# Kernel tuning notes

Measured on AMD Instinct MI355X. Metric: run time of the kernel, lower is better.

The kernel has to match this reference:

```python
import jax, jax.numpy as jnp
import numpy as np

N = 16384      # nodes
E = 131072     # edges
L = 256        # latent size
H = 256        # mlp hidden size
S = 4          # message passing steps
OUT = 128      # decoder node output size
EPS = 1e-6     # flax LayerNorm epsilon


def _mlp(x, W0, b0, W1, b1):
    h = jax.nn.relu(x @ W0 + b0)
    return h @ W1 + b1


def _mlp_ln(x, W0, b0, W1, b1, ls, lb):
    y = _mlp(x, W0, b0, W1, b1)
    mu = y.mean(-1, keepdims=True)
    var = ((y - mu) ** 2).mean(-1, keepdims=True)
    return (y - mu) * jax.lax.rsqrt(var + EPS) * ls + lb


def setup_inputs() -> dict:
    key = jax.random.key(0)
    ks = iter(jax.random.split(key, 64))
    std = 0.02

    def w(shape):
        return jax.random.normal(next(ks), shape, dtype=jnp.float32) * std

    inp = {
        'node_feats': jax.random.normal(next(ks), (N, 3), dtype=jnp.float32),
        'edge_feats': jax.random.normal(next(ks), (E, 4), dtype=jnp.float32),
        'senders': jax.random.randint(next(ks), (E,), 0, N, dtype=jnp.int32),
        'receivers': jax.random.randint(next(ks), (E,), 0, N, dtype=jnp.int32),
        # node embedder MLP (3 -> H -> L) + LayerNorm
        'en_W0': w((3, H)), 'en_b0': jnp.zeros((H,)), 'en_W1': w((H, L)), 'en_b1': jnp.zeros((L,)),
        'en_ls': jnp.ones((L,)), 'en_lb': jnp.zeros((L,)),
        # edge embedder MLP (4 -> H -> L) + LayerNorm
        'ee_W0': w((4, H)), 'ee_b0': jnp.zeros((H,)), 'ee_W1': w((H, L)), 'ee_b1': jnp.zeros((L,)),
        'ee_ls': jnp.ones((L,)), 'ee_lb': jnp.zeros((L,)),
        # processor edge MLPs, stacked over S steps (3L -> H -> L) + LN
        'pe_W0': w((S, 3 * L, H)), 'pe_b0': jnp.zeros((S, H)), 'pe_W1': w((S, H, L)), 'pe_b1': jnp.zeros((S, L)),
        'pe_ls': jnp.ones((S, L)), 'pe_lb': jnp.zeros((S, L)),
        # processor node MLPs, stacked over S steps (2L -> H -> L) + LN
        'pn_W0': w((S, 2 * L, H)), 'pn_b0': jnp.zeros((S, H)), 'pn_W1': w((S, H, L)), 'pn_b1': jnp.zeros((S, L)),
        'pn_ls': jnp.ones((S, L)), 'pn_lb': jnp.zeros((S, L)),
        # node decoder MLP (L -> H -> OUT), no LayerNorm
        'dn_W0': w((L, H)), 'dn_b0': jnp.zeros((H,)), 'dn_W1': w((H, OUT)), 'dn_b1': jnp.zeros((OUT,)),
    }
    return inp


def reference(node_feats, edge_feats, senders, receivers,
              en_W0, en_b0, en_W1, en_b1, en_ls, en_lb,
              ee_W0, ee_b0, ee_W1, ee_b1, ee_ls, ee_lb,
              pe_W0, pe_b0, pe_W1, pe_b1, pe_ls, pe_lb,
              pn_W0, pn_b0, pn_W1, pn_b1, pn_ls, pn_lb,
              dn_W0, dn_b0, dn_W1, dn_b1):
    # Embed raw node/edge features into latent space.
    nodes = _mlp_ln(node_feats, en_W0, en_b0, en_W1, en_b1, en_ls, en_lb)   # [N, L]
    edges = _mlp_ln(edge_feats, ee_W0, ee_b0, ee_W1, ee_b1, ee_ls, ee_lb)   # [E, L]

    def step(carry, p):
        nodes, edges = carry
        (eW0, eb0, eW1, eb1, els, elb, nW0, nb0, nW1, nb1, nls, nlb) = p
        # Edge update: MLP on [edge, sender_node, receiver_node].
        ein = jnp.concatenate([edges, nodes[senders], nodes[receivers]], axis=-1)  # [E, 3L]
        new_e = _mlp_ln(ein, eW0, eb0, eW1, eb1, els, elb)                          # [E, L]
        # Aggregate new edge messages into receiver nodes (segment_sum).
        agg = jax.ops.segment_sum(new_e, receivers, num_segments=N)                # [N, L]
        # Node update: MLP on [node, aggregated messages].
        nin = jnp.concatenate([nodes, agg], axis=-1)                                # [N, 2L]
        new_n = _mlp_ln(nin, nW0, nb0, nW1, nb1, nls, nlb)                          # [N, L]
        # Residual connections (as in DeepTypedGraphNet processor).
        return (nodes + new_n, edges + new_e), None

    (nodes, edges), _ = jax.lax.scan(
        step, (nodes, edges),
        (pe_W0, pe_b0, pe_W1, pe_b1, pe_ls, pe_lb,
         pn_W0, pn_b0, pn_W1, pn_b1, pn_ls, pn_lb))

    # Decoder on nodes (no LayerNorm on the output head).
    out = _mlp(nodes, dn_W0, dn_b0, dn_W1, dn_b1)  # [N, OUT]
    return out
```

## Files before the change

kernel.cpp:

```cpp
#include <hip/hip_runtime.h>
#include <hip/hip_bf16.h>

#define NN 16384
#define NE 131072
#define L 256
#define SSTEPS 4
#define OUTD 128

typedef __attribute__((ext_vector_type(8))) short bf16x8;
typedef __attribute__((ext_vector_type(4))) float f32x4;

typedef const unsigned __attribute__((address_space(1)))* as1_u32p;
typedef unsigned __attribute__((address_space(3)))* as3_u32p;

__device__ __forceinline__ void gload16(const void* g, void* lds) {
  __builtin_amdgcn_global_load_lds((as1_u32p)g, (as3_u32p)lds, 16, 0, 0);
}

__device__ __forceinline__ short f2bs(float f) {
  unsigned u = __builtin_bit_cast(unsigned, f);
  u = (u + 0x7fffu + ((u >> 16) & 1u)) >> 16;
  return (short)u;
}
__device__ __forceinline__ float bs2f(short s) {
  unsigned u = ((unsigned)(unsigned short)s) << 16;
  return __builtin_bit_cast(float, u);
}
__device__ __forceinline__ unsigned cvt_pk_bf16(float lo, float hi) {
  unsigned r;
  asm("v_cvt_pk_bf16_f32 %0, %1, %2" : "=v"(r) : "v"(lo), "v"(hi));
  return r;
}
__device__ __forceinline__ bf16x8 pack_bf16x8(const float v[8]) {
  union { unsigned u[4]; bf16x8 b; } r;
#pragma unroll
  for (int k = 0; k < 4; ++k) r.u[k] = cvt_pk_bf16(v[2 * k], v[2 * k + 1]);
  return r.b;
}

__device__ __forceinline__ void store_tile(short* hs, int l, int mi, int nb,
                                           f32x4 v) {
  const int lm = l & 15, g = l >> 4;
#pragma unroll
  for (int i = 0; i < 4; ++i) {
    const float part = __shfl_xor(v[i], 1);
    if ((l & 1) == 0) {
      const int row = mi * 16 + g * 4 + i;
      const int col = nb + lm;
      const int off = (row * 512 + col * 2) ^ ((row & 7) << 4);
      *(unsigned*)((char*)hs + off) = cvt_pk_bf16(v[i], part);
    }
  }
}

template <int MI, int NT, int KC, int AST>
__device__ __forceinline__ void gemm_lds(const short* __restrict__ Wp,
                                         int Ncols, const short* hs, int n0,
                                         int l, f32x4 acc[MI][NT]) {
  const int lm = l & 15, g = l >> 4;
#pragma unroll
  for (int kc = 0; kc < KC; ++kc) {
    bf16x8 a[MI];
#pragma unroll
    for (int mi = 0; mi < MI; ++mi) {
      const int row = mi * 16 + lm;
      const int off = (row * AST + kc * 64 + g * 16) ^ ((row & 7) << 4);
      a[mi] = *(const bf16x8*)((const char*)hs + off);
    }
#pragma unroll
    for (int ni = 0; ni < NT; ++ni) {
      const int n = n0 + ni * 16 + lm;
      bf16x8 b = *(const bf16x8*)(Wp + ((size_t)kc * Ncols + n) * 32 + g * 8);
#pragma unroll
      for (int mi = 0; mi < MI; ++mi)
        acc[mi][ni] =
            __builtin_amdgcn_mfma_f32_16x16x32_bf16(a[mi], b, acc[mi][ni], 0, 0, 0);
    }
  }
}

__global__ void pack_w(const float* __restrict__ src, short* __restrict__ dst,
                       int K, int N, int cnt) {
  const size_t total = (size_t)K * N * cnt;
  for (size_t i = (size_t)blockIdx.x * blockDim.x + threadIdx.x; i < total;
       i += (size_t)gridDim.x * blockDim.x) {
    const size_t mat = i / ((size_t)K * N);
    const int rem = (int)(i - mat * (size_t)K * N);
    const int k = rem / N, n = rem - k * N;
    dst[mat * (size_t)K * N + ((size_t)(k >> 5) * N + n) * 32 + (k & 31)] =
        f2bs(src[i]);
  }
}

__global__ void pack_w0_pad(const float* __restrict__ src,
                            short* __restrict__ dst, int Kreal) {
  const int i = blockIdx.x * 256 + threadIdx.x;
  if (i >= 256 * 32) return;
  const int n = i >> 5, k = i & 31;
  dst[n * 32 + k] = (k < Kreal) ? f2bs(src[k * 256 + n]) : (short)0;
}

__device__ __forceinline__ void stage_tile256(const short* __restrict__ src0,
                                              short* As, int w, int l) {
#pragma unroll
  for (int i = 0; i < 4; ++i) {
    const int rbase = w * 8 + i * 2;
    const int r = rbase + (l >> 5);
    const int boff = ((l & 31) * 16) ^ ((r & 7) << 4);
    gload16((const char*)(src0 + (size_t)r * L) + boff, As + rbase * 256);
  }
}

__device__ __forceinline__ void stage_tile512(const short* __restrict__ a_src,
                                              const short* __restrict__ b_src,
                                              short* As, int w, int l, int n0) {
#pragma unroll
  for (int i = 0; i < 8; ++i) {
    const int r = w * 8 + i;
    const int cb = (l * 16) ^ ((r & 7) << 4);
    const int cs = cb >> 1;
    const short* src = (cs < 256)
                           ? a_src + (size_t)(n0 + r) * L + cs
                           : b_src + (size_t)(n0 + r) * L + (cs - 256);
    gload16(src, As + r * 512);
  }
}

__global__ void csr_hist(const int* __restrict__ recv, int* __restrict__ deg) {
  const int e = blockIdx.x * 256 + threadIdx.x;
  atomicAdd(&deg[recv[e]], 1);
}
__global__ __launch_bounds__(256) void csr_scan(const int* __restrict__ deg,
                                                int* __restrict__ start,
                                                int* __restrict__ cursor) {
  __shared__ int part[256];
  const int t = threadIdx.x;
  int s = 0;
  for (int i = 0; i < NN / 256; ++i) s += deg[t * (NN / 256) + i];
  part[t] = s;
  __syncthreads();
  if (t == 0) {
    int acc = 0;
    for (int i = 0; i < 256; ++i) {
      const int v = part[i];
      part[i] = acc;
      acc += v;
    }
  }
  __syncthreads();
  int acc = part[t];
  for (int i = 0; i < NN / 256; ++i) {
    const int n = t * (NN / 256) + i;
    start[n] = acc;
    cursor[n] = acc;
    acc += deg[n];
  }
  if (t == 255) start[NN] = acc;
}
__global__ void csr_scatter(const int* __restrict__ recv,
                            int* __restrict__ cursor, int* __restrict__ elist) {
  const int e = blockIdx.x * 256 + threadIdx.x;
  const int p = atomicAdd(&cursor[recv[e]], 1);
  elist[p] = e;
}
__global__ void csr_sort(const int* __restrict__ start, int* __restrict__ elist) {
  const int n = blockIdx.x * blockDim.x + threadIdx.x;
  if (n >= NN) return;
  const int b = start[n], e = start[n + 1];
  for (int i = b + 1; i < e; ++i) {
    const int v = elist[i];
    int j = i - 1;
    while (j >= b && elist[j] > v) {
      elist[j + 1] = elist[j];
      --j;
    }
    elist[j + 1] = v;
  }
}

__global__ __launch_bounds__(256) void agg_gather(
    const short* __restrict__ new_e, const int* __restrict__ start,
    const int* __restrict__ elist, short* __restrict__ agg_b) {
  const int t = threadIdx.x, w = t >> 6, l = t & 63;
  const int half = l >> 5, lc = l & 31;
  const int n0 = blockIdx.x * 64;
  for (int i = 0; i < 8; ++i) {
    const int n = n0 + w * 16 + i * 2 + half;
    const int b = start[n], e = start[n + 1];
    float acc[8] = {0.f, 0.f, 0.f, 0.f, 0.f, 0.f, 0.f, 0.f};
#pragma unroll 2
    for (int j = b; j < e; ++j) {
      const int eid = elist[j];
      const bf16x8 v = *(const bf16x8*)(new_e + (size_t)eid * L + lc * 8);
#pragma unroll
      for (int k = 0; k < 8; ++k) acc[k] += bs2f(v[k]);
    }
    *(bf16x8*)(agg_b + (size_t)n * L + lc * 8) = pack_bf16x8(acc);
  }
}

__device__ __forceinline__ void ln_row(const short* smem, int row, int seg,
                                       const float lsv[16], const float lbv[16],
                                       float ne[16]) {
  const int off0 = (row * 512 + seg * 16) ^ ((row & 7) << 4);
  const int off1 = (row * 512 + 256 + seg * 16) ^ ((row & 7) << 4);
  const bf16x8 y0 = *(const bf16x8*)((const char*)smem + off0);
  const bf16x8 y1 = *(const bf16x8*)((const char*)smem + off1);
  float v[16];
#pragma unroll
  for (int k = 0; k < 8; ++k) {
    v[k] = bs2f(y0[k]);
    v[8 + k] = bs2f(y1[k]);
  }
  float s = 0.f;
#pragma unroll
  for (int k = 0; k < 16; ++k) s += v[k];
#pragma unroll
  for (int o = 1; o < 16; o <<= 1) s += __shfl_xor(s, o);
  const float mu = s * (1.f / 256.f);
  float sq = 0.f;
#pragma unroll
  for (int k = 0; k < 16; ++k) {
    const float d = v[k] - mu;
    sq += d * d;
  }
#pragma unroll
  for (int o = 1; o < 16; o <<= 1) sq += __shfl_xor(sq, o);
  const float rstd = rsqrtf(sq * (1.f / 256.f) + 1e-6f);
#pragma unroll
  for (int k = 0; k < 16; ++k) ne[k] = (v[k] - mu) * rstd * lsv[k] + lbv[k];
}

__device__ __forceinline__ void load16(const float* __restrict__ p, int seg,
                                       float d[16]) {
  const float4 a0 = *(const float4*)(p + seg * 8);
  const float4 a1 = *(const float4*)(p + seg * 8 + 4);
  const float4 a2 = *(const float4*)(p + 128 + seg * 8);
  const float4 a3 = *(const float4*)(p + 128 + seg * 8 + 4);
  d[0] = a0.x; d[1] = a0.y; d[2] = a0.z; d[3] = a0.w;
  d[4] = a1.x; d[5] = a1.y; d[6] = a1.z; d[7] = a1.w;
  d[8] = a2.x; d[9] = a2.y; d[10] = a2.z; d[11] = a2.w;
  d[12] = a3.x; d[13] = a3.y; d[14] = a3.z; d[15] = a3.w;
}

__global__ __launch_bounds__(256, 4) void proj_mfma(
    const short* __restrict__ nodes_b, const short* __restrict__ Wfull,
    short* __restrict__ NSb, short* __restrict__ NRb) {
  __shared__ char smem[16384];
  short* As = (short*)smem;
  const int t = threadIdx.x, w = t >> 6, l = t & 63;
  const int tr = t >> 4, seg = t & 15;
  const int n0 = blockIdx.x * 32;
  const short* Wp = Wfull + (size_t)(8 + blockIdx.y * 8) * 256 * 32;
  short* out = blockIdx.y ? NRb : NSb;

  stage_tile256(nodes_b + (size_t)n0 * L, As, w, l);
  __syncthreads();

  f32x4 acc[2][4] = {};
  gemm_lds<2, 4, 8, 512>(Wp, L, As, w * 64, l, acc);
  __syncthreads();
#pragma unroll
  for (int ni = 0; ni < 4; ++ni)
#pragma unroll
    for (int mi = 0; mi < 2; ++mi)
      store_tile(As, l, mi, w * 64 + ni * 16, acc[mi][ni]);
  __syncthreads();

#pragma unroll
  for (int p = 0; p < 2; ++p) {
    const int row = p * 16 + tr;
    const int off0 = (row * 512 + seg * 16) ^ ((row & 7) << 4);
    const int off1 = (row * 512 + 256 + seg * 16) ^ ((row & 7) << 4);
    const bf16x8 y0 = *(const bf16x8*)((const char*)As + off0);
    const bf16x8 y1 = *(const bf16x8*)((const char*)As + off1);
    *(bf16x8*)(out + (size_t)(n0 + row) * L + seg * 8) = y0;
    *(bf16x8*)(out + (size_t)(n0 + row) * L + 128 + seg * 8) = y1;
  }
}

__global__ __launch_bounds__(256, 3) void edge_step_mfma(
    const short* __restrict__ NSb, const short* __restrict__ NRb,
    short* __restrict__ edges_b, short* __restrict__ new_e,
    const int* __restrict__ senders, const int* __restrict__ receivers,
    const short* __restrict__ W0p, const float* __restrict__ b0,
    const short* __restrict__ W1p, const float* __restrict__ b1,
    const float* __restrict__ ls, const float* __restrict__ lb) {
  __shared__ char smem[49152];
  float* nsrf = (float*)smem;
  short* As = (short*)(smem + 32768);
  short* yb = (short*)smem;
  const int t = threadIdx.x, w = t >> 6, l = t & 63;
  const int lm = l & 15, g = l >> 4;
  const int tr = t >> 4, seg = t & 15;
  const int e0 = blockIdx.x * 32;

  const int sn0 = senders[e0 + tr], rc0 = receivers[e0 + tr];
  const int sn1 = senders[e0 + 16 + tr], rc1 = receivers[e0 + 16 + tr];
  stage_tile256(edges_b + (size_t)e0 * L, As, w, l);
  __syncthreads();

  bf16x8 gn[2][2], gr[2][2];
  {
    const short* p0 = NSb + (size_t)sn0 * L + seg * 8;
    gn[0][0] = *(const bf16x8*)p0;
    gn[0][1] = *(const bf16x8*)(p0 + 128);
    const short* p1 = NSb + (size_t)sn1 * L + seg * 8;
    gn[1][0] = *(const bf16x8*)p1;
    gn[1][1] = *(const bf16x8*)(p1 + 128);
    const short* q0 = NRb + (size_t)rc0 * L + seg * 8;
    gr[0][0] = *(const bf16x8*)q0;
    gr[0][1] = *(const bf16x8*)(q0 + 128);
    const short* q1 = NRb + (size_t)rc1 * L + seg * 8;
    gr[1][0] = *(const bf16x8*)q1;
    gr[1][1] = *(const bf16x8*)(q1 + 128);
  }

  f32x4 acc[2][4] = {};
  gemm_lds<2, 4, 8, 512>(W0p, L, As, w * 64, l, acc);

  bf16x8 old0[2], old1[2];
#pragma unroll
  for (int p = 0; p < 2; ++p) {
    const int row = p * 16 + tr;
    old0[p] = *(const bf16x8*)((const char*)As +
                               ((row * 512 + seg * 16) ^ ((row & 7) << 4)));
    old1[p] = *(const bf16x8*)((const char*)As +
                               ((row * 512 + 256 + seg * 16) ^ ((row & 7) << 4)));
  }

#pragma unroll
  for (int p = 0; p < 2; ++p) {
    const int row = p * 16 + tr;
    float s[16];
#pragma unroll
    for (int k = 0; k < 8; ++k) {
      s[k] = bs2f(gn[p][0][k]) + bs2f(gr[p][0][k]);
      s[8 + k] = bs2f(gn[p][1][k]) + bs2f(gr[p][1][k]);
    }
    float* d = nsrf + row * 256 + seg * 8;
    *(float4*)d = make_float4(s[0], s[1], s[2], s[3]);
    *(float4*)(d + 4) = make_float4(s[4], s[5], s[6], s[7]);
    float* d2 = nsrf + row * 256 + 128 + seg * 8;
    *(float4*)d2 = make_float4(s[8], s[9], s[10], s[11]);
    *(float4*)(d2 + 4) = make_float4(s[12], s[13], s[14], s[15]);
  }
  __syncthreads();

#pragma unroll
  for (int ni = 0; ni < 4; ++ni) {
    const float bia = b0[w * 64 + ni * 16 + lm];
    const int col = w * 64 + ni * 16 + lm;
#pragma unroll
    for (int mi = 0; mi < 2; ++mi) {
      f32x4 v = acc[mi][ni];
#pragma unroll
      for (int i = 0; i < 4; ++i) {
        const int row = mi * 16 + g * 4 + i;
        v[i] = fmaxf(v[i] + bia + nsrf[row * 256 + col], 0.f);
      }
      store_tile(As, l, mi, w * 64 + ni * 16, v);
    }
  }
  __syncthreads();

  f32x4 acc2[2][4] = {};
  gemm_lds<2, 4, 8, 512>(W1p, L, As, w * 64, l, acc2);
  __syncthreads();

#pragma unroll
  for (int ni = 0; ni < 4; ++ni) {
    const float bia = b1[w * 64 + ni * 16 + lm];
#pragma unroll
    for (int mi = 0; mi < 2; ++mi) {
      f32x4 v = acc2[mi][ni];
#pragma unroll
      for (int i = 0; i < 4; ++i) v[i] += bia;
      store_tile(yb, l, mi, w * 64 + ni * 16, v);
    }
  }
  __syncthreads();

  float lsv[16], lbv[16];
  load16(ls, seg, lsv);
  load16(lb, seg, lbv);
#pragma unroll
  for (int p = 0; p < 2; ++p) {
    const int row = p * 16 + tr;
    float ne[16];
    ln_row(yb, row, seg, lsv, lbv, ne);
    const size_t e = (size_t)(e0 + row);
    *(bf16x8*)(new_e + e * L + seg * 8) = pack_bf16x8(ne);
    *(bf16x8*)(new_e + e * L + 128 + seg * 8) = pack_bf16x8(ne + 8);
    float r0[8], r1[8];
#pragma unroll
    for (int k = 0; k < 8; ++k) {
      r0[k] = bs2f(old0[p][k]) + ne[k];
      r1[k] = bs2f(old1[p][k]) + ne[8 + k];
    }
    *(bf16x8*)(edges_b + e * L + seg * 8) = pack_bf16x8(r0);
    *(bf16x8*)(edges_b + e * L + 128 + seg * 8) = pack_bf16x8(r1);
  }
}

__global__ __launch_bounds__(256, 4) void node_step_mfma(
    float* __restrict__ nodes_f, short* __restrict__ nodes_b,
    const short* __restrict__ agg_b, const short* __restrict__ W0p,
    const float* __restrict__ b0, const short* __restrict__ W1p,
    const float* __restrict__ b1, const float* __restrict__ ls,
    const float* __restrict__ lb) {
  __shared__ char smem[32768];
  short* As = (short*)smem;
  short* hb = (short*)smem;
  short* yb = (short*)(smem + 16384);
  const int t = threadIdx.x, w = t >> 6, l = t & 63;
  const int lm = l & 15;
  const int tr = t >> 4, seg = t & 15;
  const int n0 = blockIdx.x * 32;

  stage_tile512(nodes_b, agg_b, As, w, l, n0);
  __syncthreads();

  f32x4 acc[2][4] = {};
  gemm_lds<2, 4, 16, 1024>(W0p, L, As, w * 64, l, acc);
  __syncthreads();

#pragma unroll
  for (int ni = 0; ni < 4; ++ni) {
    const float bia = b0[w * 64 + ni * 16 + lm];
#pragma unroll
    for (int mi = 0; mi < 2; ++mi) {
      f32x4 v = acc[mi][ni];
#pragma unroll
      for (int i = 0; i < 4; ++i) v[i] = fmaxf(v[i] + bia, 0.f);
      store_tile(hb, l, mi, w * 64 + ni * 16, v);
    }
  }
  __syncthreads();

  f32x4 acc2[2][4] = {};
  gemm_lds<2, 4, 8, 512>(W1p, L, hb, w * 64, l, acc2);
  __syncthreads();
#pragma unroll
  for (int ni = 0; ni < 4; ++ni) {
    const float bia = b1[w * 64 + ni * 16 + lm];
#pragma unroll
    for (int mi = 0; mi < 2; ++mi) {
      f32x4 v = acc2[mi][ni];
#pragma unroll
      for (int i = 0; i < 4; ++i) v[i] += bia;
      store_tile(yb, l, mi, w * 64 + ni * 16, v);
    }
  }
  __syncthreads();

  float lsv[16], lbv[16];
  load16(ls, seg, lsv);
  load16(lb, seg, lbv);
#pragma unroll
  for (int p = 0; p < 2; ++p) {
    const int row = p * 16 + tr;
    float ne[16];
    ln_row(yb, row, seg, lsv, lbv, ne);
    const size_t n = (size_t)(n0 + row);
    float* nf = nodes_f + n * L;
    float fv[16];
    load16(nf, seg, fv);
    float nv[16];
#pragma unroll
    for (int k = 0; k < 16; ++k) nv[k] = fv[k] + ne[k];
    *(float4*)(nf + seg * 8) = make_float4(nv[0], nv[1], nv[2], nv[3]);
    *(float4*)(nf + seg * 8 + 4) = make_float4(nv[4], nv[5], nv[6], nv[7]);
    *(float4*)(nf + 128 + seg * 8) = make_float4(nv[8], nv[9], nv[10], nv[11]);
    *(float4*)(nf + 128 + seg * 8 + 4) = make_float4(nv[12], nv[13], nv[14], nv[15]);
    *(bf16x8*)(nodes_b + n * L + seg * 8) = pack_bf16x8(nv);
    *(bf16x8*)(nodes_b + n * L + 128 + seg * 8) = pack_bf16x8(nv + 8);
  }
}

template <int K1, bool WF32>
__global__ __launch_bounds__(256) void embed_mfma(
    const float* __restrict__ x, const short* __restrict__ W0p,
    const float* __restrict__ b0, const short* __restrict__ W1p,
    const float* __restrict__ b1, const float* __restrict__ ls,
    const float* __restrict__ lb, float* __restrict__ dst_f,
    short* __restrict__ dst_b) {
  __shared__ short hs[64 * 256];
  __shared__ short xsb[64 * 32];
  const int t = threadIdx.x, w = t >> 6, l = t & 63;
  const int lm = l & 15, g = l >> 4;
  const int tr = t >> 4, seg = t & 15;
  const int r0 = blockIdx.x * 64;

  if (t < 64) {
    const float* xr = x + (size_t)(r0 + t) * K1;
    float v[8] = {0.f, 0.f, 0.f, 0.f, 0.f, 0.f, 0.f, 0.f};
#pragma unroll
    for (int k = 0; k < K1; ++k) v[k] = xr[k];
    bf16x8 z;
#pragma unroll
    for (int k = 0; k < 8; ++k) z[k] = 0;
    char* rb = (char*)xsb + t * 64;
    *(bf16x8*)(rb + (0 ^ ((t & 3) << 4))) = pack_bf16x8(v);
#pragma unroll
    for (int gi = 1; gi < 4; ++gi) *(bf16x8*)(rb + ((gi * 16) ^ ((t & 3) << 4))) = z;
  }
  __syncthreads();

  f32x4 acc[4][4] = {};
  {
    bf16x8 a[4];
#pragma unroll
    for (int mi = 0; mi < 4; ++mi) {
      const int row = mi * 16 + lm;
      a[mi] = *(const bf16x8*)((const char*)xsb + row * 64 +
                               ((g * 16) ^ ((row & 3) << 4)));
    }
#pragma unroll
    for (int ni = 0; ni < 4; ++ni) {
      const int n = w * 64 + ni * 16 + lm;
      bf16x8 b = *(const bf16x8*)(W0p + n * 32 + g * 8);
#pragma unroll
      for (int mi = 0; mi < 4; ++mi)
        acc[mi][ni] =
            __builtin_amdgcn_mfma_f32_16x16x32_bf16(a[mi], b, acc[mi][ni], 0, 0, 0);
    }
  }
#pragma unroll
  for (int ni = 0; ni < 4; ++ni) {
    const float bia = b0[w * 64 + ni * 16 + lm];
#pragma unroll
    for (int mi = 0; mi < 4; ++mi) {
      f32x4 v = acc[mi][ni];
#pragma unroll
      for (int i = 0; i < 4; ++i) v[i] = fmaxf(v[i] + bia, 0.f);
      store_tile(hs, l, mi, w * 64 + ni * 16, v);
    }
  }
  __syncthreads();

  f32x4 acc2[4][4] = {};
  gemm_lds<4, 4, 8, 512>(W1p, L, hs, w * 64, l, acc2);
  __syncthreads();
#pragma unroll
  for (int ni = 0; ni < 4; ++ni) {
    const float bia = b1[w * 64 + ni * 16 + lm];
#pragma unroll
    for (int mi = 0; mi < 4; ++mi) {
      f32x4 v = acc2[mi][ni];
#pragma unroll
      for (int i = 0; i < 4; ++i) v[i] += bia;
      store_tile(hs, l, mi, w * 64 + ni * 16, v);
    }
  }
  __syncthreads();

  float lsv[16], lbv[16];
  load16(ls, seg, lsv);
  load16(lb, seg, lbv);
#pragma unroll
  for (int p = 0; p < 4; ++p) {
    const int row = p * 16 + tr;
    float ne[16];
    ln_row(hs, row, seg, lsv, lbv, ne);
    const size_t n = (size_t)(r0 + row);
    *(bf16x8*)(dst_b + n * L + seg * 8) = pack_bf16x8(ne);
    *(bf16x8*)(dst_b + n * L + 128 + seg * 8) = pack_bf16x8(ne + 8);
    if (WF32) {
      float* df = dst_f + n * L;
      *(float4*)(df + seg * 8) = make_float4(ne[0], ne[1], ne[2], ne[3]);
      *(float4*)(df + seg * 8 + 4) = make_float4(ne[4], ne[5], ne[6], ne[7]);
      *(float4*)(df + 128 + seg * 8) = make_float4(ne[8], ne[9], ne[10], ne[11]);
      *(float4*)(df + 128 + seg * 8 + 4) =
          make_float4(ne[12], ne[13], ne[14], ne[15]);
    }
  }
}

__global__ __launch_bounds__(256) void decoder_mfma(
    const short* __restrict__ nodes_b, const short* __restrict__ W0p,
    const float* __restrict__ b0, const short* __restrict__ W1p,
    const float* __restrict__ b1, float* __restrict__ out) {
  __shared__ short hs[64 * 256];
  const int t = threadIdx.x, w = t >> 6, l = t & 63;
  const int lm = l & 15, g = l >> 4;
  const int n0 = blockIdx.x * 64;

  const short* baseA[4];
#pragma unroll
  for (int mi = 0; mi < 4; ++mi)
    baseA[mi] = nodes_b + (size_t)(n0 + mi * 16 + lm) * L;

  f32x4 acc[4][4] = {};
#pragma unroll
  for (int kc = 0; kc < 8; ++kc) {
    const int koff = kc * 32 + g * 8;
    bf16x8 a[4];
#pragma unroll
    for (int mi = 0; mi < 4; ++mi) a[mi] = *(const bf16x8*)(baseA[mi] + koff);
#pragma unroll
    for (int ni = 0; ni < 4; ++ni) {
      const int n = w * 64 + ni * 16 + lm;
      bf16x8 b = *(const bf16x8*)(W0p + ((size_t)kc * L + n) * 32 + g * 8);
#pragma unroll
      for (int mi = 0; mi < 4; ++mi)
        acc[mi][ni] = __builtin_amdgcn_mfma_f32_16x16x32_bf16(a[mi], b,
                                                             acc[mi][ni],
                                                             0, 0, 0);
    }
  }
#pragma unroll
  for (int ni = 0; ni < 4; ++ni) {
    const float bia = b0[w * 64 + ni * 16 + lm];
#pragma unroll
    for (int mi = 0; mi < 4; ++mi) {
      f32x4 v = acc[mi][ni];
#pragma unroll
      for (int i = 0; i < 4; ++i) v[i] = fmaxf(v[i] + bia, 0.f);
      store_tile(hs, l, mi, w * 64 + ni * 16, v);
    }
  }
  __syncthreads();

  f32x4 acc2[4][2] = {};
  gemm_lds<4, 2, 8, 512>(W1p, OUTD, hs, w * 32, l, acc2);

  float b14[2];
#pragma unroll
  for (int ni = 0; ni < 2; ++ni) b14[ni] = b1[w * 32 + ni * 16 + lm];
#pragma unroll
  for (int mi = 0; mi < 4; ++mi)
#pragma unroll
    for (int ni = 0; ni < 2; ++ni)
#pragma unroll
      for (int i = 0; i < 4; ++i) {
        const int row = n0 + mi * 16 + g * 4 + i;
        const int col = w * 32 + ni * 16 + lm;
        out[(size_t)row * OUTD + col] = acc2[mi][ni][i] + b14[ni];
      }
}

extern "C" void kernel_launch(void* const* d_in, const int* in_sizes, int n_in,
                              void* d_out, int out_size, void* d_ws,
                              size_t ws_size, hipStream_t stream) {
  const float* node_feats = (const float*)d_in[0];
  const float* edge_feats = (const float*)d_in[1];
  const int* senders = (const int*)d_in[2];
  const int* receivers = (const int*)d_in[3];
  auto f = [&](int i) { return (const float*)d_in[i]; };

  char* p = (char*)d_ws;
  auto alloc = [&](size_t bytes) {
    char* q = p;
    p += (bytes + 255) & ~(size_t)255;
    return q;
  };
  float* nodes_f = (float*)alloc((size_t)NN * L * 4);
  short* nodes_b = (short*)alloc((size_t)NN * L * 2);
  short* edges_b = (short*)alloc((size_t)NE * L * 2);
  short* new_e = (short*)alloc((size_t)NE * L * 2);
  short* agg_b = (short*)alloc((size_t)NN * L * 2);
  short* NSb = (short*)alloc((size_t)NN * L * 2);
  short* NRb = (short*)alloc((size_t)NN * L * 2);
  int* deg = (int*)alloc((size_t)NN * 4);
  int* start = (int*)alloc((size_t)(NN + 16) * 4);
  int* cursor = (int*)alloc((size_t)NN * 4);
  int* elist = (int*)alloc((size_t)NE * 4);
  short* en_W0p = (short*)alloc(256 * 32 * 2);
  short* ee_W0p = (short*)alloc(256 * 32 * 2);
  short* en_W1p = (short*)alloc(65536 * 2);
  short* ee_W1p = (short*)alloc(65536 * 2);
  short* pe_W0p = (short*)alloc((size_t)4 * 768 * 256 * 2);
  short* pe_W1p = (short*)alloc((size_t)4 * 65536 * 2);
  short* pn_W0p = (short*)alloc((size_t)4 * 512 * 256 * 2);
  short* pn_W1p = (short*)alloc((size_t)4 * 65536 * 2);
  short* dn_W0p = (short*)alloc(65536 * 2);
  short* dn_W1p = (short*)alloc(32768 * 2);

  hipMemsetAsync(deg, 0, (size_t)NN * 4, stream);
  csr_hist<<<NE / 256, 256, 0, stream>>>(receivers, deg);
  csr_scan<<<1, 256, 0, stream>>>(deg, start, cursor);
  csr_scatter<<<NE / 256, 256, 0, stream>>>(receivers, cursor, elist);
  csr_sort<<<NN / 256, 256, 0, stream>>>(start, elist);

  pack_w0_pad<<<32, 256, 0, stream>>>(f(4), en_W0p, 3);
  pack_w0_pad<<<32, 256, 0, stream>>>(f(10), ee_W0p, 4);
  pack_w<<<256, 256, 0, stream>>>(f(6), en_W1p, 256, 256, 1);
  pack_w<<<256, 256, 0, stream>>>(f(12), ee_W1p, 256, 256, 1);
  pack_w<<<1024, 256, 0, stream>>>(f(16), pe_W0p, 768, 256, 4);
  pack_w<<<512, 256, 0, stream>>>(f(18), pe_W1p, 256, 256, 4);
  pack_w<<<1024, 256, 0, stream>>>(f(22), pn_W0p, 512, 256, 4);
  pack_w<<<512, 256, 0, stream>>>(f(24), pn_W1p, 256, 256, 4);
  pack_w<<<256, 256, 0, stream>>>(f(28), dn_W0p, 256, 256, 1);
  pack_w<<<128, 256, 0, stream>>>(f(30), dn_W1p, 256, 128, 1);

  embed_mfma<3, true><<<NN / 64, 256, 0, stream>>>(
      node_feats, en_W0p, f(5), en_W1p, f(7), f(8), f(9), nodes_f, nodes_b);
  embed_mfma<4, false><<<NE / 64, 256, 0, stream>>>(
      edge_feats, ee_W0p, f(11), ee_W1p, f(13), f(14), f(15), nullptr, edges_b);

  for (int s = 0; s < SSTEPS; ++s) {
    const short* W0s = pe_W0p + (size_t)s * 768 * 256;
    proj_mfma<<<dim3(NN / 32, 2), 256, 0, stream>>>(nodes_b, W0s, NSb, NRb);
    edge_step_mfma<<<NE / 32, 256, 0, stream>>>(
        NSb, NRb, edges_b, new_e, senders, receivers, W0s,
        f(17) + (size_t)s * 256, pe_W1p + (size_t)s * 65536,
        f(19) + (size_t)s * 256, f(20) + (size_t)s * 256,
        f(21) + (size_t)s * 256);
    agg_gather<<<NN / 64, 256, 0, stream>>>(new_e, start, elist, agg_b);
    node_step_mfma<<<NN / 32, 256, 0, stream>>>(
        nodes_f, nodes_b, agg_b, pn_W0p + (size_t)s * 512 * 256,
        f(23) + (size_t)s * 256, pn_W1p + (size_t)s * 65536,
        f(25) + (size_t)s * 256, f(26) + (size_t)s * 256,
        f(27) + (size_t)s * 256);
  }

  decoder_mfma<<<NN / 64, 256, 0, stream>>>(nodes_b, dn_W0p, f(29), dn_W1p,
                                            f(31), (float*)d_out);
}
```

Before: 952.7 us.

## Fuse next-step node projections into node step, shrink edge LDS, widen agg grid

The node-step kernel now also computes the sender and receiver projections for the next message-passing step from the freshly updated bf16 nodes held in LDS. This removes the separate proj_mfma launch and its re-read of the node array for steps after the first. The edge step keeps the gathered sender+receiver sum in bf16 rather than f32, which halves its shared memory and lets the launch bound rise from 3 to 4 blocks. The bf16 sum adds some rounding, and agg_gather now gives each half-wave a single node for more parallelism.

```diff
diff --git a/kernel.cpp b/kernel.cpp
--- a/kernel.cpp
+++ b/kernel.cpp
@@ -183,20 +183,17 @@
     const int* __restrict__ elist, short* __restrict__ agg_b) {
   const int t = threadIdx.x, w = t >> 6, l = t & 63;
   const int half = l >> 5, lc = l & 31;
-  const int n0 = blockIdx.x * 64;
-  for (int i = 0; i < 8; ++i) {
-    const int n = n0 + w * 16 + i * 2 + half;
-    const int b = start[n], e = start[n + 1];
-    float acc[8] = {0.f, 0.f, 0.f, 0.f, 0.f, 0.f, 0.f, 0.f};
+  const int n = blockIdx.x * 8 + w * 2 + half;
+  const int b = start[n], e = start[n + 1];
+  float acc[8] = {0.f, 0.f, 0.f, 0.f, 0.f, 0.f, 0.f, 0.f};
 #pragma unroll 2
-    for (int j = b; j < e; ++j) {
-      const int eid = elist[j];
-      const bf16x8 v = *(const bf16x8*)(new_e + (size_t)eid * L + lc * 8);
-#pragma unroll
-      for (int k = 0; k < 8; ++k) acc[k] += bs2f(v[k]);
-    }
-    *(bf16x8*)(agg_b + (size_t)n * L + lc * 8) = pack_bf16x8(acc);
-  }
+  for (int j = b; j < e; ++j) {
+    const int eid = elist[j];
+    const bf16x8 v = *(const bf16x8*)(new_e + (size_t)eid * L + lc * 8);
+#pragma unroll
+    for (int k = 0; k < 8; ++k) acc[k] += bs2f(v[k]);
+  }
+  *(bf16x8*)(agg_b + (size_t)n * L + lc * 8) = pack_bf16x8(acc);
 }
 
 __device__ __forceinline__ void ln_row(const short* smem, int row, int seg,
@@ -272,24 +269,23 @@
     const int row = p * 16 + tr;
     const int off0 = (row * 512 + seg * 16) ^ ((row & 7) << 4);
     const int off1 = (row * 512 + 256 + seg * 16) ^ ((row & 7) << 4);
-    const bf16x8 y0 = *(const bf16x8*)((const char*)As + off0);
-    const bf16x8 y1 = *(const bf16x8*)((const char*)As + off1);
-    *(bf16x8*)(out + (size_t)(n0 + row) * L + seg * 8) = y0;
-    *(bf16x8*)(out + (size_t)(n0 + row) * L + 128 + seg * 8) = y1;
-  }
-}
-
-__global__ __launch_bounds__(256, 3) void edge_step_mfma(
+    *(bf16x8*)(out + (size_t)(n0 + row) * L + seg * 8) =
+        *(const bf16x8*)((const char*)As + off0);
+    *(bf16x8*)(out + (size_t)(n0 + row) * L + 128 + seg * 8) =
+        *(const bf16x8*)((const char*)As + off1);
+  }
+}
+
+__global__ __launch_bounds__(256, 4) void edge_step_mfma(
     const short* __restrict__ NSb, const short* __restrict__ NRb,
     short* __restrict__ edges_b, short* __restrict__ new_e,
     const int* __restrict__ senders, const int* __restrict__ receivers,
     const short* __restrict__ W0p, const float* __restrict__ b0,
     const short* __restrict__ W1p, const float* __restrict__ b1,
     const float* __restrict__ ls, const float* __restrict__ lb) {
-  __shared__ char smem[49152];
-  float* nsrf = (float*)smem;
-  short* As = (short*)(smem + 32768);
-  short* yb = (short*)smem;
+  __shared__ char smem[32768];
+  short* As = (short*)smem;
+  short* nsrB = (short*)(smem + 16384);
   const int t = threadIdx.x, w = t >> 6, l = t & 63;
   const int lm = l & 15, g = l >> 4;
   const int tr = t >> 4, seg = t & 15;
@@ -338,12 +334,10 @@
       s[k] = bs2f(gn[p][0][k]) + bs2f(gr[p][0][k]);
       s[8 + k] = bs2f(gn[p][1][k]) + bs2f(gr[p][1][k]);
     }
-    float* d = nsrf + row * 256 + seg * 8;
-    *(float4*)d = make_float4(s[0], s[1], s[2], s[3]);
-    *(float4*)(d + 4) = make_float4(s[4], s[5], s[6], s[7]);
-    float* d2 = nsrf + row * 256 + 128 + seg * 8;
-    *(float4*)d2 = make_float4(s[8], s[9], s[10], s[11]);
-    *(float4*)(d2 + 4) = make_float4(s[12], s[13], s[14], s[15]);
+    const int off0 = (row * 512 + seg * 16) ^ ((row & 7) << 4);
+    const int off1 = (row * 512 + 256 + seg * 16) ^ ((row & 7) << 4);
+    *(bf16x8*)((char*)nsrB + off0) = pack_bf16x8(s);
+    *(bf16x8*)((char*)nsrB + off1) = pack_bf16x8(s + 8);
   }
   __syncthreads();
 
@@ -357,7 +351,9 @@
 #pragma unroll
       for (int i = 0; i < 4; ++i) {
         const int row = mi * 16 + g * 4 + i;
-        v[i] = fmaxf(v[i] + bia + nsrf[row * 256 + col], 0.f);
+        const int noff = (row * 512 + col * 2) ^ ((row & 7) << 4);
+        v[i] = fmaxf(v[i] + bia + bs2f(*(const short*)((const char*)nsrB + noff)),
+                     0.f);
       }
       store_tile(As, l, mi, w * 64 + ni * 16, v);
     }
@@ -366,8 +362,6 @@
 
   f32x4 acc2[2][4] = {};
   gemm_lds<2, 4, 8, 512>(W1p, L, As, w * 64, l, acc2);
-  __syncthreads();
-
 #pragma unroll
   for (int ni = 0; ni < 4; ++ni) {
     const float bia = b1[w * 64 + ni * 16 + lm];
@@ -376,7 +370,7 @@
       f32x4 v = acc2[mi][ni];
 #pragma unroll
       for (int i = 0; i < 4; ++i) v[i] += bia;
-      store_tile(yb, l, mi, w * 64 + ni * 16, v);
+      store_tile(nsrB, l, mi, w * 64 + ni * 16, v);
     }
   }
   __syncthreads();
@@ -388,7 +382,7 @@
   for (int p = 0; p < 2; ++p) {
     const int row = p * 16 + tr;
     float ne[16];
-    ln_row(yb, row, seg, lsv, lbv, ne);
+    ln_row(nsrB, row, seg, lsv, lbv, ne);
     const size_t e = (size_t)(e0 + row);
     *(bf16x8*)(new_e + e * L + seg * 8) = pack_bf16x8(ne);
     *(bf16x8*)(new_e + e * L + 128 + seg * 8) = pack_bf16x8(ne + 8);
@@ -408,7 +402,9 @@
     const short* __restrict__ agg_b, const short* __restrict__ W0p,
     const float* __restrict__ b0, const short* __restrict__ W1p,
     const float* __restrict__ b1, const float* __restrict__ ls,
-    const float* __restrict__ lb) {
+    const float* __restrict__ lb, const short* __restrict__ W0nS,
+    const short* __restrict__ W0nR, short* __restrict__ NSb,
+    short* __restrict__ NRb) {
   __shared__ char smem[32768];
   short* As = (short*)smem;
   short* hb = (short*)smem;
@@ -473,8 +469,60 @@
     *(float4*)(nf + seg * 8 + 4) = make_float4(nv[4], nv[5], nv[6], nv[7]);
     *(float4*)(nf + 128 + seg * 8) = make_float4(nv[8], nv[9], nv[10], nv[11]);
     *(float4*)(nf + 128 + seg * 8 + 4) = make_float4(nv[12], nv[13], nv[14], nv[15]);
-    *(bf16x8*)(nodes_b + n * L + seg * 8) = pack_bf16x8(nv);
-    *(bf16x8*)(nodes_b + n * L + 128 + seg * 8) = pack_bf16x8(nv + 8);
+    const bf16x8 nb0 = pack_bf16x8(nv);
+    const bf16x8 nb1 = pack_bf16x8(nv + 8);
+    *(bf16x8*)(nodes_b + n * L + seg * 8) = nb0;
+    *(bf16x8*)(nodes_b + n * L + 128 + seg * 8) = nb1;
+    const int off0 = (row * 512 + seg * 16) ^ ((row & 7) << 4);
+    const int off1 = (row * 512 + 256 + seg * 16) ^ ((row & 7) << 4);
+    *(bf16x8*)((char*)hb + off0) = nb0;
+    *(bf16x8*)((char*)hb + off1) = nb1;
+  }
+
+  if (W0nS == nullptr) return;
+  __syncthreads();
+
+  {
+    f32x4 pa[2][4] = {};
+    gemm_lds<2, 4, 8, 512>(W0nS, L, hb, w * 64, l, pa);
+#pragma unroll
+    for (int ni = 0; ni < 4; ++ni)
+#pragma unroll
+      for (int mi = 0; mi < 2; ++mi)
+        store_tile(yb, l, mi, w * 64 + ni * 16, pa[mi][ni]);
+    __syncthreads();
+#pragma unroll
+    for (int p = 0; p < 2; ++p) {
+      const int row = p * 16 + tr;
+      const int off0 = (row * 512 + seg * 16) ^ ((row & 7) << 4);
+      const int off1 = (row * 512 + 256 + seg * 16) ^ ((row & 7) << 4);
+      *(bf16x8*)(NSb + (size_t)(n0 + row) * L + seg * 8) =
+          *(const bf16x8*)((const char*)yb + off0);
+      *(bf16x8*)(NSb + (size_t)(n0 + row) * L + 128 + seg * 8) =
+          *(const bf16x8*)((const char*)yb + off1);
+    }
+  }
+  __syncthreads();
+
+  {
+    f32x4 pa[2][4] = {};
+    gemm_lds<2, 4, 8, 512>(W0nR, L, hb, w * 64, l, pa);
+#pragma unroll
+    for (int ni = 0; ni < 4; ++ni)
+#pragma unroll
+      for (int mi = 0; mi < 2; ++mi)
+        store_tile(yb, l, mi, w * 64 + ni * 16, pa[mi][ni]);
+    __syncthreads();
+#pragma unroll
+    for (int p = 0; p < 2; ++p) {
+      const int row = p * 16 + tr;
+      const int off0 = (row * 512 + seg * 16) ^ ((row & 7) << 4);
+      const int off1 = (row * 512 + 256 + seg * 16) ^ ((row & 7) << 4);
+      *(bf16x8*)(NRb + (size_t)(n0 + row) * L + seg * 8) =
+          *(const bf16x8*)((const char*)yb + off0);
+      *(bf16x8*)(NRb + (size_t)(n0 + row) * L + 128 + seg * 8) =
+          *(const bf16x8*)((const char*)yb + off1);
+    }
   }
 }
 
@@ -701,18 +749,22 @@
 
   for (int s = 0; s < SSTEPS; ++s) {
     const short* W0s = pe_W0p + (size_t)s * 768 * 256;
-    proj_mfma<<<dim3(NN / 32, 2), 256, 0, stream>>>(nodes_b, W0s, NSb, NRb);
+    if (s == 0)
+      proj_mfma<<<dim3(NN / 32, 2), 256, 0, stream>>>(nodes_b, W0s, NSb, NRb);
     edge_step_mfma<<<NE / 32, 256, 0, stream>>>(
         NSb, NRb, edges_b, new_e, senders, receivers, W0s,
         f(17) + (size_t)s * 256, pe_W1p + (size_t)s * 65536,
         f(19) + (size_t)s * 256, f(20) + (size_t)s * 256,
         f(21) + (size_t)s * 256);
-    agg_gather<<<NN / 64, 256, 0, stream>>>(new_e, start, elist, agg_b);
+    agg_gather<<<NN / 8, 256, 0, stream>>>(new_e, start, elist, agg_b);
+    const short* W0n = (s + 1 < SSTEPS) ? pe_W0p + (size_t)(s + 1) * 768 * 256
+                                        : nullptr;
     node_step_mfma<<<NN / 32, 256, 0, stream>>>(
         nodes_f, nodes_b, agg_b, pn_W0p + (size_t)s * 512 * 256,
         f(23) + (size_t)s * 256, pn_W1p + (size_t)s * 65536,
         f(25) + (size_t)s * 256, f(26) + (size_t)s * 256,
-        f(27) + (size_t)s * 256);
+        f(27) + (size_t)s * 256, W0n ? W0n + (size_t)8 * 256 * 32 : nullptr,
+        W0n ? W0n + (size_t)16 * 256 * 32 : nullptr, NSb, NRb);
   }
 
   decoder_mfma<<<NN / 64, 256, 0, stream>>>(nodes_b, dn_W0p, f(29), dn_W1p,
```

Result: faster. 814.5 us (-14.5%).
